# Kernel tuning notes

Measured on AMD Instinct MI355X. Metric: run time of the kernel, lower is better.

The kernel has to match this reference:

```python
import jax, jax.numpy as jnp
import numpy as np

BATCH = 16384
NUM_IN = 4096
NUM_OUT = 1024
NNZ = 262144
BN_EPS = 1e-3  # keras BatchNormalization default epsilon


def setup_inputs() -> dict:
    key = jax.random.key(0)
    ks = jax.random.split(key, 6)
    x = jax.random.normal(ks[0], (BATCH, NUM_IN), dtype=jnp.float32)
    sp_values = jax.random.normal(ks[1], (NNZ,), dtype=jnp.float32)
    gamma = jnp.ones((NUM_IN,), dtype=jnp.float32)
    beta = jnp.zeros((NUM_IN,), dtype=jnp.float32)
    moving_mean = jax.random.normal(ks[2], (NUM_IN,), dtype=jnp.float32)
    # positive moving variance in [0.5, 1.5)
    moving_var = jax.random.uniform(ks[3], (NUM_IN,), dtype=jnp.float32, minval=0.5, maxval=1.5)
    sp_rows = jax.random.randint(ks[4], (NNZ,), 0, NUM_IN, dtype=jnp.int32)
    sp_cols = jax.random.randint(ks[5], (NNZ,), 0, NUM_OUT, dtype=jnp.int32)
    return {
        "x": x,
        "sp_values": sp_values,
        "gamma": gamma,
        "beta": beta,
        "moving_mean": moving_mean,
        "moving_var": moving_var,
        "sp_rows": sp_rows,
        "sp_cols": sp_cols,
    }


def reference(x, sp_values, gamma, beta, moving_mean, moving_var, sp_rows, sp_cols):
    # BatchNorm (inference mode, moving statistics), fused elementwise
    h = (x - moving_mean) * (gamma * jax.lax.rsqrt(moving_var + BN_EPS)) + beta
    # Scatter the fixed-index sparse weights into a small dense [NUM_IN, NUM_OUT]
    # matrix (16 MB), then a single dense GEMM — honors SparseTensor semantics
    # (duplicate indices accumulate) while staying GEMM-efficient.
    W = jnp.zeros((NUM_IN, NUM_OUT), dtype=x.dtype).at[sp_rows, sp_cols].add(sp_values)
    return h @ W  # [BATCH, NUM_OUT]
```

## Files before the change

kernel.cpp:

```cpp
#include <hip/hip_runtime.h>
#include <hip/hip_bf16.h>

#define BATCH   16384
#define NUM_IN  4096
#define NUM_OUT 1024
#define NNZ     262144
#define BN_EPS  1e-3f

typedef __attribute__((ext_vector_type(8))) short   short8;
typedef __attribute__((ext_vector_type(4))) float   f32x4;
typedef __attribute__((ext_vector_type(4))) unsigned int u32x4;

typedef __attribute__((address_space(3))) void        lds_void_t;
typedef const __attribute__((address_space(1))) void  g_void_t;

__device__ inline unsigned short f2bf(float f) {
    unsigned int u = __builtin_bit_cast(unsigned int, f);
    u += 0x7fffu + ((u >> 16) & 1u);
    return (unsigned short)(u >> 16);
}

__global__ void k_zero(f32x4* __restrict__ p) {
    p[(size_t)blockIdx.x * 256 + threadIdx.x] = f32x4{0.f, 0.f, 0.f, 0.f};
}

__global__ void k_scatter(const float* __restrict__ v, const int* __restrict__ r,
                          const int* __restrict__ c, float* __restrict__ wtf) {
    int i = blockIdx.x * 256 + threadIdx.x;
    atomicAdd(&wtf[(size_t)c[i] * NUM_IN + r[i]], v[i]);
}

__global__ void k_wprep(const float* __restrict__ wtf, const float* __restrict__ gamma,
                        const float* __restrict__ beta, const float* __restrict__ mean,
                        const float* __restrict__ var, unsigned short* __restrict__ wtb,
                        float* __restrict__ bias) {
    const int n = blockIdx.x;
    const int t = threadIdx.x;
    float acc = 0.f;
    for (int k = t; k < NUM_IN; k += 256) {
        float w = wtf[(size_t)n * NUM_IN + k];
        float s = gamma[k] * rsqrtf(var[k] + BN_EPS);
        wtb[(size_t)n * NUM_IN + k] = f2bf(w * s);
        acc += (beta[k] - mean[k] * s) * w;
    }
    #pragma unroll
    for (int o = 32; o; o >>= 1) acc += __shfl_down(acc, o, 64);
    __shared__ float red[4];
    if ((t & 63) == 0) red[t >> 6] = acc;
    __syncthreads();
    if (t == 0) bias[n] = red[0] + red[1] + red[2] + red[3];
}

#define BM 128
#define BN 256
#define BK 32
#define KTILES (NUM_IN / BK)
#define ABUF 16384
#define BBUF 16384
#define LDS_B_OFF 65536

__global__ __launch_bounds__(512, 2) void k_gemm(const float* __restrict__ x,
                                                 const unsigned short* __restrict__ wt,
                                                 const float* __restrict__ bias,
                                                 float* __restrict__ out) {
    __shared__ __align__(128) char lds[131072];

    const int bid = blockIdx.x;
    const int swz = (bid & 7) * 64 + (bid >> 3);
    const int m0 = (swz >> 2) * BM;
    const int n0 = (swz & 3) * BN;

    const int t    = threadIdx.x;
    const int lane = t & 63;
    const int wid  = t >> 6;
    const int wm   = wid >> 1;
    const int wn   = wid & 1;

    const int arow0 = t >> 3;
    const int akb   = (t & 7) * 16;
    const int brow0 = t >> 2;
    const int bkb   = (t & 3) * 16;

    const char* xb = (const char*)x;
    const char* wb = (const char*)wt;

    auto stage = [&](int kt) {
        const int buf = kt & 3;
        #pragma unroll
        for (int q = 0; q < 2; ++q) {
            int row = q * 64 + arow0;
            int src = (m0 + row) * (NUM_IN * 4) + kt * (BK * 4) + (akb ^ ((row & 7) << 4));
            __builtin_amdgcn_global_load_lds((g_void_t*)(xb + src),
                (lds_void_t*)(lds + buf * ABUF + q * 8192 + t * 16), 16, 0, 0);
        }
        #pragma unroll
        for (int q = 0; q < 2; ++q) {
            int row = q * 128 + brow0;
            int src = (n0 + row) * (NUM_IN * 2) + kt * (BK * 2) + (bkb ^ ((row & 3) << 4));
            __builtin_amdgcn_global_load_lds((g_void_t*)(wb + src),
                (lds_void_t*)(lds + LDS_B_OFF + buf * BBUF + q * 8192 + t * 16), 16, 0, 0);
        }
    };

    f32x4 acc[2][8] = {};

    const int arf = wm * 32 + (lane & 15);
    const int a_kb = (lane >> 4) * 32;
    const int brf = wn * 128 + (lane & 15);
    const int b_kb = (lane >> 4) * 16;

    auto compute = [&](int kt) {
        const char* A = lds + (kt & 3) * ABUF;
        const char* B = lds + LDS_B_OFF + (kt & 3) * BBUF;
        f32x4 ar[2][2];
        short8 bfr[8];
        #pragma unroll
        for (int m = 0; m < 2; ++m) {
            int row = arf + m * 16;
            int s = (row & 7) << 4;
            ar[m][0] = *(const f32x4*)(A + row * 128 + (a_kb ^ s));
            ar[m][1] = *(const f32x4*)(A + row * 128 + ((a_kb + 16) ^ s));
        }
        #pragma unroll
        for (int j = 0; j < 8; ++j) {
            int row = brf + j * 16;
            bfr[j] = *(const short8*)(B + row * 64 + (b_kb ^ ((row & 3) << 4)));
        }
        short8 af[2];
        #pragma unroll
        for (int m = 0; m < 2; ++m) {
            const unsigned int* f0 = (const unsigned int*)&ar[m][0];
            const unsigned int* f1 = (const unsigned int*)&ar[m][1];
            u32x4 p;
            p[0] = __builtin_amdgcn_perm(f0[1], f0[0], 0x07060302u);
            p[1] = __builtin_amdgcn_perm(f0[3], f0[2], 0x07060302u);
            p[2] = __builtin_amdgcn_perm(f1[1], f1[0], 0x07060302u);
            p[3] = __builtin_amdgcn_perm(f1[3], f1[2], 0x07060302u);
            af[m] = __builtin_bit_cast(short8, p);
        }
        __builtin_amdgcn_s_setprio(1);
        #pragma unroll
        for (int m = 0; m < 2; ++m)
            #pragma unroll
            for (int j = 0; j < 8; ++j)
                acc[m][j] = __builtin_amdgcn_mfma_f32_16x16x32_bf16(af[m], bfr[j],
                                                                    acc[m][j], 0, 0, 0);
        __builtin_amdgcn_s_setprio(0);
    };

    stage(0); stage(1); stage(2);
    asm volatile("s_waitcnt vmcnt(8)" ::: "memory");
    __builtin_amdgcn_s_barrier();
    __builtin_amdgcn_sched_barrier(0);

    for (int kt = 0; kt < KTILES - 3; ++kt) {
        stage(kt + 3);
        compute(kt);
        asm volatile("s_waitcnt vmcnt(8)" ::: "memory");
        __builtin_amdgcn_s_barrier();
        __builtin_amdgcn_sched_barrier(0);
    }
    compute(KTILES - 3);
    asm volatile("s_waitcnt vmcnt(4)" ::: "memory");
    __builtin_amdgcn_s_barrier();
    __builtin_amdgcn_sched_barrier(0);
    compute(KTILES - 2);
    asm volatile("s_waitcnt vmcnt(0)" ::: "memory");
    __builtin_amdgcn_s_barrier();
    __builtin_amdgcn_sched_barrier(0);
    compute(KTILES - 1);

    float bj[8];
    #pragma unroll
    for (int j = 0; j < 8; ++j) bj[j] = bias[n0 + wn * 128 + j * 16 + (lane & 15)];
    const int mb = m0 + wm * 32 + (lane >> 4) * 4;
    const int nb = n0 + wn * 128 + (lane & 15);
    #pragma unroll
    for (int m = 0; m < 2; ++m)
        #pragma unroll
        for (int j = 0; j < 8; ++j)
            #pragma unroll
            for (int r = 0; r < 4; ++r)
                out[(size_t)(mb + m * 16 + r) * NUM_OUT + (nb + j * 16)] =
                    acc[m][j][r] + bj[j];
}

extern "C" void kernel_launch(void* const* d_in, const int* in_sizes, int n_in,
                              void* d_out, int out_size, void* d_ws, size_t ws_size,
                              hipStream_t stream) {
    const float* x     = (const float*)d_in[0];
    const float* spv   = (const float*)d_in[1];
    const float* gamma = (const float*)d_in[2];
    const float* beta  = (const float*)d_in[3];
    const float* mean  = (const float*)d_in[4];
    const float* var   = (const float*)d_in[5];
    const int*   rows  = (const int*)d_in[6];
    const int*   cols  = (const int*)d_in[7];
    float* out = (float*)d_out;

    float* wtf = (float*)d_out;
    unsigned short* wtb = (unsigned short*)d_ws;
    float* bias = (float*)((char*)d_ws + (size_t)NUM_IN * NUM_OUT * sizeof(unsigned short));

    hipLaunchKernelGGL(k_zero, dim3((NUM_IN * NUM_OUT / 4) / 256), dim3(256), 0, stream,
                       (f32x4*)wtf);
    hipLaunchKernelGGL(k_scatter, dim3(NNZ / 256), dim3(256), 0, stream,
                       spv, rows, cols, wtf);
    hipLaunchKernelGGL(k_wprep, dim3(NUM_OUT), dim3(256), 0, stream,
                       wtf, gamma, beta, mean, var, wtb, bias);
    hipLaunchKernelGGL(k_gemm, dim3((BATCH / BM) * (NUM_OUT / BN)), dim3(512), 0, stream,
                       x, wtb, bias, out);
}
```

Measured before the change: 226.2 us.

## Double GEMM M-tile to 256 with triple-buffered LDS pipeline

Doubles the GEMM block tile along M from 128 to 256 rows, so each wave holds 4x8 MFMA accumulators and each B fragment is reused across twice as many A rows. This cuts repeated reads of the bf16 weight matrix and halves the grid to 256 blocks. To fit the larger A tile, the LDS pipeline drops from four buffers to three, for about 144 KB of LDS. The B swizzle also changes to use (row>>1)&3 to reduce LDS bank conflicts. Risks: at most one block per CU fits in that LDS, the halved grid leaves less parallelism, and the larger accumulator set under launch_bounds(512,2) may cause register pressure or spills.

```diff
diff --git a/kernel.cpp b/kernel.cpp
--- a/kernel.cpp
+++ b/kernel.cpp
@@ -51,22 +51,22 @@
     if (t == 0) bias[n] = red[0] + red[1] + red[2] + red[3];
 }
 
-#define BM 128
+#define BM 256
 #define BN 256
 #define BK 32
 #define KTILES (NUM_IN / BK)
-#define ABUF 16384
-#define BBUF 16384
-#define LDS_B_OFF 65536
+#define ABYTES 32768
+#define BBYTES 16384
+#define PBUF   49152
 
 __global__ __launch_bounds__(512, 2) void k_gemm(const float* __restrict__ x,
                                                  const unsigned short* __restrict__ wt,
                                                  const float* __restrict__ bias,
                                                  float* __restrict__ out) {
-    __shared__ __align__(128) char lds[131072];
+    __shared__ __align__(128) char lds[3 * PBUF];
 
     const int bid = blockIdx.x;
-    const int swz = (bid & 7) * 64 + (bid >> 3);
+    const int swz = (bid & 7) * 32 + (bid >> 3);
     const int m0 = (swz >> 2) * BM;
     const int n0 = (swz & 3) * BN;
 
@@ -76,61 +76,57 @@
     const int wm   = wid >> 1;
     const int wn   = wid & 1;
 
-    const int arow0 = t >> 3;
-    const int akb   = (t & 7) * 16;
-    const int brow0 = t >> 2;
-    const int bkb   = (t & 3) * 16;
-
     const char* xb = (const char*)x;
     const char* wb = (const char*)wt;
 
-    auto stage = [&](int kt) {
-        const int buf = kt & 3;
+    const int a_r0 = t >> 3, a_c = (t & 7) * 16;
+    const int b_r0 = t >> 2, b_c = (t & 3) * 16;
+
+    auto stage = [&](int kt, int buf) {
+        char* base = lds + buf * PBUF;
+        #pragma unroll
+        for (int q = 0; q < 4; ++q) {
+            int row = q * 64 + a_r0;
+            size_t src = (size_t)(m0 + row) * (NUM_IN * 4) + kt * (BK * 4)
+                       + (a_c ^ ((row & 7) << 4));
+            __builtin_amdgcn_global_load_lds((g_void_t*)(xb + src),
+                (lds_void_t*)(base + q * 8192 + t * 16), 16, 0, 0);
+        }
         #pragma unroll
         for (int q = 0; q < 2; ++q) {
-            int row = q * 64 + arow0;
-            int src = (m0 + row) * (NUM_IN * 4) + kt * (BK * 4) + (akb ^ ((row & 7) << 4));
-            __builtin_amdgcn_global_load_lds((g_void_t*)(xb + src),
-                (lds_void_t*)(lds + buf * ABUF + q * 8192 + t * 16), 16, 0, 0);
-        }
-        #pragma unroll
-        for (int q = 0; q < 2; ++q) {
-            int row = q * 128 + brow0;
-            int src = (n0 + row) * (NUM_IN * 2) + kt * (BK * 2) + (bkb ^ ((row & 3) << 4));
+            int row = q * 128 + b_r0;
+            size_t src = (size_t)(n0 + row) * (NUM_IN * 2) + kt * (BK * 2)
+                       + (b_c ^ (((row >> 1) & 3) << 4));
             __builtin_amdgcn_global_load_lds((g_void_t*)(wb + src),
-                (lds_void_t*)(lds + LDS_B_OFF + buf * BBUF + q * 8192 + t * 16), 16, 0, 0);
+                (lds_void_t*)(base + ABYTES + q * 8192 + t * 16), 16, 0, 0);
         }
     };
 
-    f32x4 acc[2][8] = {};
-
-    const int arf = wm * 32 + (lane & 15);
-    const int a_kb = (lane >> 4) * 32;
-    const int brf = wn * 128 + (lane & 15);
-    const int b_kb = (lane >> 4) * 16;
-
-    auto compute = [&](int kt) {
-        const char* A = lds + (kt & 3) * ABUF;
-        const char* B = lds + LDS_B_OFF + (kt & 3) * BBUF;
-        f32x4 ar[2][2];
+    f32x4 acc[4][8] = {};
+
+    const int a_row0 = wm * 64 + (lane & 15);
+    const int a_kb   = (lane >> 4) * 32;
+    const int b_row0 = wn * 128 + (lane & 15);
+    const int b_kb   = (lane >> 4) * 16;
+
+    auto compute = [&](int buf) {
+        const char* A = lds + buf * PBUF;
+        const char* B = A + ABYTES;
         short8 bfr[8];
         #pragma unroll
-        for (int m = 0; m < 2; ++m) {
-            int row = arf + m * 16;
+        for (int j = 0; j < 8; ++j) {
+            int row = b_row0 + j * 16;
+            bfr[j] = *(const short8*)(B + row * 64 + (b_kb ^ (((row >> 1) & 3) << 4)));
+        }
+        short8 af[4];
+        #pragma unroll
+        for (int m = 0; m < 4; ++m) {
+            int row = a_row0 + m * 16;
             int s = (row & 7) << 4;
-            ar[m][0] = *(const f32x4*)(A + row * 128 + (a_kb ^ s));
-            ar[m][1] = *(const f32x4*)(A + row * 128 + ((a_kb + 16) ^ s));
-        }
-        #pragma unroll
-        for (int j = 0; j < 8; ++j) {
-            int row = brf + j * 16;
-            bfr[j] = *(const short8*)(B + row * 64 + (b_kb ^ ((row & 3) << 4)));
-        }
-        short8 af[2];
-        #pragma unroll
-        for (int m = 0; m < 2; ++m) {
-            const unsigned int* f0 = (const unsigned int*)&ar[m][0];
-            const unsigned int* f1 = (const unsigned int*)&ar[m][1];
+            f32x4 lo = *(const f32x4*)(A + row * 128 + (a_kb ^ s));
+            f32x4 hi = *(const f32x4*)(A + row * 128 + ((a_kb + 16) ^ s));
+            const unsigned int* f0 = (const unsigned int*)&lo;
+            const unsigned int* f1 = (const unsigned int*)&hi;
             u32x4 p;
             p[0] = __builtin_amdgcn_perm(f0[1], f0[0], 0x07060302u);
             p[1] = __builtin_amdgcn_perm(f0[3], f0[2], 0x07060302u);
@@ -140,7 +136,7 @@
         }
         __builtin_amdgcn_s_setprio(1);
         #pragma unroll
-        for (int m = 0; m < 2; ++m)
+        for (int m = 0; m < 4; ++m)
             #pragma unroll
             for (int j = 0; j < 8; ++j)
                 acc[m][j] = __builtin_amdgcn_mfma_f32_16x16x32_bf16(af[m], bfr[j],
@@ -148,35 +144,36 @@
         __builtin_amdgcn_s_setprio(0);
     };
 
-    stage(0); stage(1); stage(2);
-    asm volatile("s_waitcnt vmcnt(8)" ::: "memory");
+    stage(0, 0);
+    stage(1, 1);
+    asm volatile("s_waitcnt vmcnt(6)" ::: "memory");
     __builtin_amdgcn_s_barrier();
     __builtin_amdgcn_sched_barrier(0);
 
-    for (int kt = 0; kt < KTILES - 3; ++kt) {
-        stage(kt + 3);
-        compute(kt);
-        asm volatile("s_waitcnt vmcnt(8)" ::: "memory");
+    int cur = 0, sb = 2;
+    for (int kt = 0; kt < KTILES - 2; ++kt) {
+        stage(kt + 2, sb);
+        compute(cur);
+        asm volatile("s_waitcnt vmcnt(6)" ::: "memory");
         __builtin_amdgcn_s_barrier();
         __builtin_amdgcn_sched_barrier(0);
+        cur = (cur == 2) ? 0 : cur + 1;
+        sb  = (sb  == 2) ? 0 : sb  + 1;
     }
-    compute(KTILES - 3);
-    asm volatile("s_waitcnt vmcnt(4)" ::: "memory");
-    __builtin_amdgcn_s_barrier();
-    __builtin_amdgcn_sched_barrier(0);
-    compute(KTILES - 2);
+    compute(cur);
+    cur = (cur == 2) ? 0 : cur + 1;
     asm volatile("s_waitcnt vmcnt(0)" ::: "memory");
     __builtin_amdgcn_s_barrier();
     __builtin_amdgcn_sched_barrier(0);
-    compute(KTILES - 1);
+    compute(cur);
 
     float bj[8];
     #pragma unroll
     for (int j = 0; j < 8; ++j) bj[j] = bias[n0 + wn * 128 + j * 16 + (lane & 15)];
-    const int mb = m0 + wm * 32 + (lane >> 4) * 4;
+    const int mb = m0 + wm * 64 + (lane >> 4) * 4;
     const int nb = n0 + wn * 128 + (lane & 15);
     #pragma unroll
-    for (int m = 0; m < 2; ++m)
+    for (int m = 0; m < 4; ++m)
         #pragma unroll
         for (int j = 0; j < 8; ++j)
             #pragma unroll
```

New measurement: 191.1 us. 15.5% less time.
